# Kernel optimization log

Measured on AMD Instinct MI355X. Metric: run time of the kernel, lower is better.

## Reference

```python
import jax, jax.numpy as jnp
import numpy as np

# Module hyperparameters (init_kwargs)
NCE_K = 256      # samples per example (col 0 = positive)
NCE_T = 0.07     # temperature
EPS = 1e-7

# Problem sizes
B = 4096         # batch
D = 128          # embedding dim
N = 1_000_000    # memory bank size


def setup_inputs() -> dict:
    key = jax.random.key(0)
    k1, k2, k3, k4 = jax.random.split(key, 4)
    x = jax.random.normal(k1, (B, D), dtype=jnp.float32)
    targets = jax.random.randint(k2, (B,), 0, N)
    memory = jax.random.normal(k3, (N, D), dtype=jnp.float32) * 0.05
    # uniform multinomial-with-replacement sampling == uniform randint
    indices = jax.random.randint(k4, (B, NCE_K), 0, N)
    return {"x": x, "targets": targets, "memory": memory, "indices": indices}


def reference(x, targets, memory, indices):
    # nce_average: overwrite column 0 with the positive index
    idx = indices.at[:, 0].set(targets)              # [B, K]
    weight = memory[idx]                              # [B, K, D] gather
    logits = jnp.einsum('bkd,bd->bk', weight, x) / NCE_T
    sims = jnp.exp(logits)                            # [B, K]
    sims = sims / jnp.sum(sims, axis=1, keepdims=True) * (NCE_K / N)

    # NCE loss: K' = nce_k - 1 noise samples per example
    Kp = NCE_K - 1
    noise = Kp / N
    lnPmt = sims[:, 0] / (sims[:, 0] + noise + EPS)   # [B]
    lnPon = noise / (sims[:, 1:] + noise + EPS)       # [B, K-1]
    loss = -(jnp.log(lnPmt).mean() + jnp.log(lnPon).sum(axis=1).mean())
    return loss
```

## Files before the change

### kernel.cpp

```cpp
#include <hip/hip_runtime.h>

#define B_SZ 4096
#define D_SZ 128
#define K_SZ 256

constexpr float INV_T    = 1.0f / 0.07f;
constexpr float NOISE    = 255.0f / 1000000.0f;
constexpr float EPS_C    = 1e-7f;
constexpr float K_OVER_N = 256.0f / 1000000.0f;

__global__ __launch_bounds__(256, 8) void nce_main(
    const float* __restrict__ x,
    const int*   __restrict__ targets,
    const float* __restrict__ memory,
    const int*   __restrict__ indices,
    float*       __restrict__ partial)
{
    __shared__ float4 s_x[D_SZ / 4];
    __shared__ float  s_red[4];

    const int b    = blockIdx.x;
    const int tid  = threadIdx.x;
    const int lane = tid & 63;
    const int wave = tid >> 6;

    if (tid < D_SZ / 4)
        s_x[tid] = ((const float4*)(x + (size_t)b * D_SZ))[tid];

    const int myidx = (tid == 0) ? targets[b]
                                 : indices[(size_t)b * K_SZ + tid];
    __syncthreads();

    const float4* __restrict__ wrow =
        (const float4*)(memory + (size_t)myidx * D_SZ);

    float a0 = 0.f, a1 = 0.f, a2 = 0.f, a3 = 0.f;
    #pragma unroll
    for (int j = 0; j < D_SZ / 4; j += 4) {
        const float4 w0 = wrow[j + 0];
        const float4 w1 = wrow[j + 1];
        const float4 w2 = wrow[j + 2];
        const float4 w3 = wrow[j + 3];
        const float4 x0 = s_x[j + 0];
        const float4 x1 = s_x[j + 1];
        const float4 x2 = s_x[j + 2];
        const float4 x3 = s_x[j + 3];
        a0 = fmaf(w0.x, x0.x, fmaf(w0.y, x0.y, fmaf(w0.z, x0.z, fmaf(w0.w, x0.w, a0))));
        a1 = fmaf(w1.x, x1.x, fmaf(w1.y, x1.y, fmaf(w1.z, x1.z, fmaf(w1.w, x1.w, a1))));
        a2 = fmaf(w2.x, x2.x, fmaf(w2.y, x2.y, fmaf(w2.z, x2.z, fmaf(w2.w, x2.w, a2))));
        a3 = fmaf(w3.x, x3.x, fmaf(w3.y, x3.y, fmaf(w3.z, x3.z, fmaf(w3.w, x3.w, a3))));
    }
    const float p = (a0 + a1) + (a2 + a3);
    const float e = expf(p * INV_T);

    float sum = e;
    #pragma unroll
    for (int m = 32; m >= 1; m >>= 1)
        sum += __shfl_xor(sum, m, 64);
    if (lane == 0) s_red[wave] = sum;
    __syncthreads();
    const float S = s_red[0] + s_red[1] + s_red[2] + s_red[3];

    const float sims = e * (K_OVER_N / S);
    float term = (tid == 0)
        ? logf(sims / (sims + NOISE + EPS_C))
        : logf(NOISE / (sims + NOISE + EPS_C));

    #pragma unroll
    for (int m = 32; m >= 1; m >>= 1)
        term += __shfl_xor(term, m, 64);
    __syncthreads();
    if (lane == 0) s_red[wave] = term;
    __syncthreads();
    if (tid == 0)
        partial[b] = s_red[0] + s_red[1] + s_red[2] + s_red[3];
}

__global__ __launch_bounds__(256) void nce_final(
    const float* __restrict__ partial, float* __restrict__ out)
{
    const int tid = threadIdx.x;
    float s = 0.0f;
    #pragma unroll
    for (int i = tid; i < B_SZ; i += 256)
        s += partial[i];
    #pragma unroll
    for (int m = 32; m >= 1; m >>= 1)
        s += __shfl_xor(s, m, 64);
    __shared__ float sr[4];
    if ((tid & 63) == 0) sr[tid >> 6] = s;
    __syncthreads();
    if (tid == 0)
        out[0] = -(sr[0] + sr[1] + sr[2] + sr[3]) / (float)B_SZ;
}

extern "C" void kernel_launch(void* const* d_in, const int* in_sizes, int n_in,
                              void* d_out, int out_size, void* d_ws, size_t ws_size,
                              hipStream_t stream) {
    const float* x       = (const float*)d_in[0];
    const int*   targets = (const int*)  d_in[1];
    const float* memory  = (const float*)d_in[2];
    const int*   indices = (const int*)  d_in[3];
    float* out     = (float*)d_out;
    float* partial = (float*)d_ws;

    nce_main<<<B_SZ, 256, 0, stream>>>(x, targets, memory, indices, partial);
    nce_final<<<1, 256, 0, stream>>>(partial, out);
}
```

Baseline: 683.1 us.

## Bin gathered samples by memory-row bucket to localize random memory-bank reads

Splits the fused per-batch kernel into a pipeline of five kernels. It zeroes the counters, then bins every (batch, sample) pair by memory row into 256-row buckets using atomics. It computes the dot products bucket by bucket, which makes the memory-bank reads mostly contiguous and lets repeated rows hit in cache, then does the softmax/log reduction from a stored exp buffer. This trades extra launches, atomic traffic and intermediate buffers, plus random reads of x, for better DRAM locality on the large gather. Buckets are capped at 1024 entries, so a heavily skewed index distribution would silently drop samples.

```diff
diff --git a/kernel.cpp b/kernel.cpp
--- a/kernel.cpp
+++ b/kernel.cpp
@@ -1,57 +1,103 @@
 #include <hip/hip_runtime.h>
 
-#define B_SZ 4096
-#define D_SZ 128
-#define K_SZ 256
+#define B_SZ   4096
+#define D_SZ   128
+#define K_SZ   256
+#define NBUCK  4096
+#define BCAP   1024
 
 constexpr float INV_T    = 1.0f / 0.07f;
 constexpr float NOISE    = 255.0f / 1000000.0f;
 constexpr float EPS_C    = 1e-7f;
 constexpr float K_OVER_N = 256.0f / 1000000.0f;
 
-__global__ __launch_bounds__(256, 8) void nce_main(
+
+__global__ __launch_bounds__(256) void zero_counters(int* __restrict__ cnt)
+{
+    const int i = blockIdx.x * 256 + threadIdx.x;
+    if (i < NBUCK) cnt[i] = 0;
+}
+
+__global__ __launch_bounds__(256, 8) void bin_samples(
+    const int* __restrict__ targets,
+    const int* __restrict__ indices,
+    int*                 __restrict__ cnt,
+    unsigned long long*  __restrict__ ent)
+{
+    const int i = blockIdx.x * 256 + threadIdx.x;
+    const int b = i >> 8;
+    const int k = i & (K_SZ - 1);
+    const int row = (k == 0) ? targets[b] : indices[i];
+    const int bu  = row >> 8;
+    const int slot = atomicAdd(&cnt[bu], 1);
+    if (slot < BCAP)
+        ent[(size_t)bu * BCAP + slot] =
+            ((unsigned long long)(unsigned)row << 32) | (unsigned)i;
+}
+
+__global__ __launch_bounds__(256, 4) void gather_dot(
     const float* __restrict__ x,
-    const int*   __restrict__ targets,
     const float* __restrict__ memory,
-    const int*   __restrict__ indices,
+    const int*                __restrict__ cnt,
+    const unsigned long long* __restrict__ ent,
+    float*       __restrict__ esims)
+{
+    const int bu = blockIdx.x;
+    const int nb = min(cnt[bu], BCAP);
+    if (nb == 0) return;
+
+    const int tid = threadIdx.x;
+    const int g   = tid >> 3;
+    const int s   = tid & 7;
+
+    for (int base = 0; base < nb; base += 32) {
+        const int e  = base + g;
+        const int ec = min(e, nb - 1);
+        const unsigned long long pk = ent[(size_t)bu * BCAP + ec];
+        const int i   = (int)(pk & 0xffffffffu);
+        const int row = (int)(pk >> 32);
+
+        const float4* __restrict__ rp =
+            (const float4*)(memory + (size_t)row * D_SZ);
+        const float4* __restrict__ xp =
+            (const float4*)(x + (size_t)(i >> 8) * D_SZ);
+
+        const float4 r0 = rp[0 * 8 + s];
+        const float4 r1 = rp[1 * 8 + s];
+        const float4 r2 = rp[2 * 8 + s];
+        const float4 r3 = rp[3 * 8 + s];
+        const float4 x0 = xp[0 * 8 + s];
+        const float4 x1 = xp[1 * 8 + s];
+        const float4 x2 = xp[2 * 8 + s];
+        const float4 x3 = xp[3 * 8 + s];
+
+        float a0 = 0.f, a1 = 0.f;
+        a0 = fmaf(r0.x, x0.x, fmaf(r0.y, x0.y, fmaf(r0.z, x0.z, fmaf(r0.w, x0.w, a0))));
+        a1 = fmaf(r1.x, x1.x, fmaf(r1.y, x1.y, fmaf(r1.z, x1.z, fmaf(r1.w, x1.w, a1))));
+        a0 = fmaf(r2.x, x2.x, fmaf(r2.y, x2.y, fmaf(r2.z, x2.z, fmaf(r2.w, x2.w, a0))));
+        a1 = fmaf(r3.x, x3.x, fmaf(r3.y, x3.y, fmaf(r3.z, x3.z, fmaf(r3.w, x3.w, a1))));
+        float p = a0 + a1;
+
+        p += __shfl_xor(p, 1, 64);
+        p += __shfl_xor(p, 2, 64);
+        p += __shfl_xor(p, 4, 64);
+
+        if (s == 0 && e < nb)
+            esims[i] = expf(p * INV_T);
+    }
+}
+
+__global__ __launch_bounds__(256, 8) void reduce_loss(
+    const float* __restrict__ esims,
     float*       __restrict__ partial)
 {
-    __shared__ float4 s_x[D_SZ / 4];
-    __shared__ float  s_red[4];
-
+    __shared__ float s_red[4];
     const int b    = blockIdx.x;
     const int tid  = threadIdx.x;
     const int lane = tid & 63;
     const int wave = tid >> 6;
 
-    if (tid < D_SZ / 4)
-        s_x[tid] = ((const float4*)(x + (size_t)b * D_SZ))[tid];
-
-    const int myidx = (tid == 0) ? targets[b]
-                                 : indices[(size_t)b * K_SZ + tid];
-    __syncthreads();
-
-    const float4* __restrict__ wrow =
-        (const float4*)(memory + (size_t)myidx * D_SZ);
-
-    float a0 = 0.f, a1 = 0.f, a2 = 0.f, a3 = 0.f;
-    #pragma unroll
-    for (int j = 0; j < D_SZ / 4; j += 4) {
-        const float4 w0 = wrow[j + 0];
-        const float4 w1 = wrow[j + 1];
-        const float4 w2 = wrow[j + 2];
-        const float4 w3 = wrow[j + 3];
-        const float4 x0 = s_x[j + 0];
-        const float4 x1 = s_x[j + 1];
-        const float4 x2 = s_x[j + 2];
-        const float4 x3 = s_x[j + 3];
-        a0 = fmaf(w0.x, x0.x, fmaf(w0.y, x0.y, fmaf(w0.z, x0.z, fmaf(w0.w, x0.w, a0))));
-        a1 = fmaf(w1.x, x1.x, fmaf(w1.y, x1.y, fmaf(w1.z, x1.z, fmaf(w1.w, x1.w, a1))));
-        a2 = fmaf(w2.x, x2.x, fmaf(w2.y, x2.y, fmaf(w2.z, x2.z, fmaf(w2.w, x2.w, a2))));
-        a3 = fmaf(w3.x, x3.x, fmaf(w3.y, x3.y, fmaf(w3.z, x3.z, fmaf(w3.w, x3.w, a3))));
-    }
-    const float p = (a0 + a1) + (a2 + a3);
-    const float e = expf(p * INV_T);
+    const float e = esims[(size_t)b * K_SZ + tid];
 
     float sum = e;
     #pragma unroll
@@ -101,9 +147,17 @@
     const int*   targets = (const int*)  d_in[1];
     const float* memory  = (const float*)d_in[2];
     const int*   indices = (const int*)  d_in[3];
-    float* out     = (float*)d_out;
-    float* partial = (float*)d_ws;
+    float* out = (float*)d_out;
 
-    nce_main<<<B_SZ, 256, 0, stream>>>(x, targets, memory, indices, partial);
+    char* ws = (char*)d_ws;
+    int*                cnt     = (int*)ws;
+    unsigned long long* ent     = (unsigned long long*)(ws + 16384);
+    float*              esims   = (float*)(ws + 16384 + (size_t)NBUCK * BCAP * 8);
+    float*              partial = esims + (size_t)B_SZ * K_SZ;
+
+    zero_counters<<<NBUCK / 256, 256, 0, stream>>>(cnt);
+    bin_samples<<<(B_SZ * K_SZ) / 256, 256, 0, stream>>>(targets, indices, cnt, ent);
+    gather_dot<<<NBUCK, 256, 0, stream>>>(x, memory, cnt, ent, esims);
+    reduce_loss<<<B_SZ, 256, 0, stream>>>(esims, partial);
     nce_final<<<1, 256, 0, stream>>>(partial, out);
 }
```

Measured after the change: 743.2 us. 1.09x slower.
